# Kernel optimization log

Measured on AMD Instinct MI355X. Metric: run time of the kernel, lower is better.

Reference implementation:

```python
import jax, jax.numpy as jnp
import numpy as np

N_NODES = 100000
BN_EPS = 1e-5


def gcn_conv(x, row, col, ew, W, b, n):
    # PyG GCNConv (normalize=True, add_self_loops=True):
    # add self loops with weight 1, symmetric deg^-1/2 normalization,
    # message = norm * (x @ W)[row], scatter-add at col (target), + bias.
    h = x @ W  # [N, F_out]
    loop = jnp.arange(n)
    row_f = jnp.concatenate([row, loop])
    col_f = jnp.concatenate([col, loop])
    ew_f = jnp.concatenate([ew, jnp.ones((n,), dtype=ew.dtype)])
    deg = jax.ops.segment_sum(ew_f, col_f, num_segments=n)  # [N]
    dis = jnp.where(deg > 0, jax.lax.rsqrt(jnp.maximum(deg, 1e-30)), 0.0)
    norm = dis[row_f] * ew_f * dis[col_f]  # [E+N]
    msg = norm[:, None] * h[row_f]  # [E+N, F_out]
    agg = jax.ops.segment_sum(msg, col_f, num_segments=n)
    return agg + b


def batchnorm(h, gamma, beta):
    mean = h.mean(axis=0)
    var = h.var(axis=0)  # biased, as torch BN training-mode normalization
    return gamma * (h - mean) * jax.lax.rsqrt(var + BN_EPS) + beta


def setup_inputs() -> dict:
    key = jax.random.key(0)
    ks = jax.random.split(key, 12)
    N, E, D = N_NODES, 3200000, 256
    x = jax.random.normal(ks[0], (N, D), dtype=jnp.float32)
    edge_index = jax.random.randint(ks[1], (2, E), 0, N, dtype=jnp.int64)
    edge_weight = jax.random.uniform(ks[2], (E,), dtype=jnp.float32)
    s = 1.0 / np.sqrt(D)
    W1 = jax.random.uniform(ks[3], (D, D), jnp.float32, -s, s)
    b1 = jnp.zeros((D,), jnp.float32)
    g1 = jnp.ones((D,), jnp.float32)
    be1 = jnp.zeros((D,), jnp.float32)
    W2 = jax.random.uniform(ks[4], (D, D), jnp.float32, -s, s)
    b2 = jnp.zeros((D,), jnp.float32)
    g2 = jnp.ones((D,), jnp.float32)
    be2 = jnp.zeros((D,), jnp.float32)
    return {"x": x, "edge_index": edge_index, "edge_weight": edge_weight,
            "W1": W1, "b1": b1, "g1": g1, "be1": be1,
            "W2": W2, "b2": b2, "g2": g2, "be2": be2}


def reference(x, edge_index, edge_weight, W1, b1, g1, be1, W2, b2, g2, be2):
    n = x.shape[0]
    row, col = edge_index[0], edge_index[1]
    h = gcn_conv(x, row, col, edge_weight, W1, b1, n)
    h = jax.nn.relu(batchnorm(h, g1, be1))
    h = gcn_conv(h, row, col, edge_weight, W2, b2, n)
    h = batchnorm(h, g2, be2)
    # in_dim == out_dim -> proj is Identity
    return jax.nn.relu(h + x)
```

## Files before the change

### kernel.cpp

```cpp
#include <hip/hip_runtime.h>
#include <hip/hip_bf16.h>

#define D 256
#define BN_EPS 1e-5f
#define CHUNK 4096
#define NPB 512
#define CAP_B 20480

typedef __attribute__((ext_vector_type(8))) short bf16x8;
typedef __attribute__((ext_vector_type(4))) float f32x4;
typedef unsigned long long ull;
typedef unsigned char uchar;

__device__ inline uint pack2_rne(float a, float b) {
    uint ua = __builtin_bit_cast(uint, a);
    ua = ua + 0x7FFFu + ((ua >> 16) & 1u);
    uint ub = __builtin_bit_cast(uint, b);
    ub = ub + 0x7FFFu + ((ub >> 16) & 1u);
    return (ua >> 16) | (ub & 0xFFFF0000u);
}
__device__ inline ushort f2bf_rne(float a) {
    uint ua = __builtin_bit_cast(uint, a);
    ua = ua + 0x7FFFu + ((ua >> 16) & 1u);
    return (ushort)(ua >> 16);
}
__device__ inline float bf2f(ushort u) {
    uint x = ((uint)u) << 16;
    return __builtin_bit_cast(float, x);
}
__device__ inline uint pack_edge(uint rowbits, uint ewbits) {
    uint b15 = (ewbits + 0x8000u) >> 16;
    return (rowbits & 0x1FFFFu) | (b15 << 17);
}
__device__ inline float edge_ew(uint e) {
    return __builtin_bit_cast(float, (e >> 17) << 16);
}

__global__ __launch_bounds__(256) void init_fast_kernel(int* __restrict__ cursor,
                                                        float* __restrict__ stats) {
    int t = threadIdx.x;
    cursor[t] = t * CAP_B;
    stats[t] = 0.f;
    stats[t + 256] = 0.f;
    stats[t + 512] = 0.f;
    stats[t + 768] = 0.f;
}

__global__ __launch_bounds__(256) void bin_kernel(const int* __restrict__ row,
                                                  const int* __restrict__ col,
                                                  const float* __restrict__ ew,
                                                  int* __restrict__ cursor,
                                                  uint2* __restrict__ bdata, int E) {
    __shared__ int h[256];
    __shared__ int base[256];
    int t = threadIdx.x;
    h[t] = 0;
    __syncthreads();
    int cb = blockIdx.x * CHUNK;
    int cols[CHUNK / 256];
#pragma unroll
    for (int i = 0; i < CHUNK / 256; ++i) {
        int e = cb + i * 256 + t;
        int c = (e < E) ? col[e] : -1;
        cols[i] = c;
        if (c >= 0) atomicAdd(&h[c >> 9], 1);
    }
    __syncthreads();
    if (h[t]) base[t] = atomicAdd(&cursor[t], h[t]);
    __syncthreads();
    h[t] = 0;
    __syncthreads();
#pragma unroll
    for (int i = 0; i < CHUNK / 256; ++i) {
        int e = cb + i * 256 + t;
        int c = cols[i];
        if (c >= 0) {
            int b = c >> 9;
            int pos = base[b] + atomicAdd(&h[b], 1);
            if (pos < (b + 1) * CAP_B) {
                uint xv = (uint)row[e] | ((uint)(c & (NPB - 1)) << 17);
                bdata[pos] = make_uint2(xv, __float_as_uint(ew[e]));
            }
        }
    }
}

__global__ __launch_bounds__(256) void final_csr_kernel(const uint2* __restrict__ bdata,
                                                        const int* __restrict__ cursor,
                                                        uint* __restrict__ csr,
                                                        int* __restrict__ offs,
                                                        int* __restrict__ cnts,
                                                        float2* __restrict__ dscale, int N) {
    __shared__ int cnt[NPB];
    __shared__ float deg[NPB];
    __shared__ int sp[256];
    int bkt = blockIdx.x;
    int t = threadIdx.x;
    int beg = bkt * CAP_B;
    int end = min(cursor[bkt], beg + CAP_B);
    cnt[t] = 0; cnt[t + 256] = 0;
    deg[t] = 0.f; deg[t + 256] = 0.f;
    __syncthreads();
    for (int i = beg + t; i < end; i += 256) {
        uint2 v = bdata[i];
        int cl = v.x >> 17;
        atomicAdd(&cnt[cl], 1);
        atomicAdd(&deg[cl], __uint_as_float(v.y));
    }
    __syncthreads();
    int a0 = cnt[2 * t], a1 = cnt[2 * t + 1];
    sp[t] = a0 + a1;
    __syncthreads();
    for (int o = 1; o < 256; o <<= 1) {
        int add = (t >= o) ? sp[t - o] : 0;
        __syncthreads();
        sp[t] += add;
        __syncthreads();
    }
    int ex = sp[t] - (a0 + a1);
    int n0 = bkt * NPB + 2 * t;
    if (n0 < N) {
        offs[n0] = beg + ex;
        cnts[n0] = a0;
        dscale[n0].x = rsqrtf(deg[2 * t] + 1.0f);
    }
    if (n0 + 1 < N) {
        offs[n0 + 1] = beg + ex + a0;
        cnts[n0 + 1] = a1;
        dscale[n0 + 1].x = rsqrtf(deg[2 * t + 1] + 1.0f);
    }
    __syncthreads();
    cnt[2 * t] = ex;
    cnt[2 * t + 1] = ex + a0;
    __syncthreads();
    for (int i = beg + t; i < end; i += 256) {
        uint2 v = bdata[i];
        int cl = v.x >> 17;
        int pos = beg + atomicAdd(&cnt[cl], 1);
        csr[pos] = pack_edge(v.x, v.y);
    }
}

__global__ __launch_bounds__(256) void count_deg_kernel(const int* __restrict__ col,
                                                        const float* __restrict__ ew,
                                                        ull* __restrict__ dg, int E) {
    int e = blockIdx.x * 256 + threadIdx.x;
    if (e < E) {
        int c = col[e];
        uint q = (uint)(ew[e] * 8388608.0f + 0.5f);
        atomicAdd(&dg[c], (1ull << 40) | (ull)q);
    }
}

__global__ __launch_bounds__(256) void dis_cnt_kernel(const ull* __restrict__ dg,
                                                      float2* __restrict__ dscale,
                                                      int* __restrict__ cnt,
                                                      int* __restrict__ cnts,
                                                      float* __restrict__ stats, int N) {
    int i = blockIdx.x * 256 + threadIdx.x;
    if (i < 1024) stats[i] = 0.0f;
    if (i < N) {
        ull g = dg[i];
        int c = (int)(g >> 40);
        cnt[i] = c;
        cnts[i] = c;
        float deg = (float)(g & ((1ull << 40) - 1)) * (1.0f / 8388608.0f);
        dscale[i].x = rsqrtf(deg + 1.0f);
    }
}

__global__ __launch_bounds__(256) void scan_reduce(const int* __restrict__ cnt,
                                                   int* __restrict__ bsum, int N) {
    __shared__ int sd[256];
    int t = threadIdx.x;
    int i = blockIdx.x * 256 + t;
    sd[t] = (i < N) ? cnt[i] : 0;
    __syncthreads();
    for (int o = 128; o > 0; o >>= 1) {
        if (t < o) sd[t] += sd[t + o];
        __syncthreads();
    }
    if (t == 0) bsum[blockIdx.x] = sd[0];
}

__global__ __launch_bounds__(512) void scan_bsum(int* __restrict__ bsum, int B) {
    __shared__ int sd[512];
    int t = threadIdx.x;
    int v = (t < B) ? bsum[t] : 0;
    sd[t] = v;
    __syncthreads();
    for (int o = 1; o < 512; o <<= 1) {
        int add = (t >= o) ? sd[t - o] : 0;
        __syncthreads();
        sd[t] += add;
        __syncthreads();
    }
    if (t < B) bsum[t] = sd[t] - v;
}

__global__ __launch_bounds__(256) void scan_final(const int* __restrict__ cnt,
                                                  const int* __restrict__ bsum,
                                                  int* __restrict__ offs,
                                                  int* __restrict__ next, int N, int E) {
    __shared__ int sd[256];
    int t = threadIdx.x;
    int i = blockIdx.x * 256 + t;
    int v = (i < N) ? cnt[i] : 0;
    sd[t] = v;
    __syncthreads();
    for (int o = 1; o < 256; o <<= 1) {
        int add = (t >= o) ? sd[t - o] : 0;
        __syncthreads();
        sd[t] += add;
        __syncthreads();
    }
    int excl = sd[t] - v + bsum[blockIdx.x];
    if (i < N) {
        offs[i] = excl;
        next[i] = excl;
    }
    if (i == 0 && blockIdx.x == 0) offs[N] = E;
}

__global__ __launch_bounds__(256) void fill_kernel(const int* __restrict__ row,
                                                   const int* __restrict__ col,
                                                   const float* __restrict__ ew,
                                                   int* __restrict__ next,
                                                   uint* __restrict__ csr, int E) {
    int e = blockIdx.x * 256 + threadIdx.x;
    if (e < E) {
        int pos = atomicAdd(&next[col[e]], 1);
        csr[pos] = pack_edge((uint)row[e], __float_as_uint(ew[e]));
    }
}

__global__ __launch_bounds__(256) void prep_wt2_kernel(const float* __restrict__ W1,
                                                       const float* __restrict__ W2,
                                                       ushort* __restrict__ Wt1,
                                                       ushort* __restrict__ Wt2) {
    __shared__ float tile[64][65];
    const float* W = blockIdx.y ? W2 : W1;
    ushort* Wt = blockIdx.y ? Wt2 : Wt1;
    int t = threadIdx.x;
    int k0 = (blockIdx.x >> 2) * 64;
    int n0 = (blockIdx.x & 3) * 64;
#pragma unroll
    for (int it = 0; it < 16; ++it) {
        int idx = it * 256 + t;
        int r = idx >> 6, c = idx & 63;
        tile[r][c] = W[(size_t)(k0 + r) * D + n0 + c];
    }
    __syncthreads();
#pragma unroll
    for (int it = 0; it < 16; ++it) {
        int idx = it * 256 + t;
        int n = idx >> 6, k = idx & 63;
        Wt[(size_t)(n0 + n) * D + k0 + k] = f2bf_rne(tile[k][n]);
    }
}

template <int MODE>
__global__ __launch_bounds__(256) void gemm_mfma(const float* __restrict__ Xf,
                                                 const ushort* __restrict__ Xb,
                                                 const float* __restrict__ stats,
                                                 const float* __restrict__ gamma,
                                                 const float* __restrict__ beta,
                                                 const ushort* __restrict__ Wt,
                                                 uchar* __restrict__ Hq,
                                                 float2* __restrict__ dscale,
                                                 int N, float invN) {
    __shared__ char wt_lds[32 * 1024];
    __shared__ float cf_lds[2][MODE ? 256 : 1];
    const int t = threadIdx.x;
    const int wv = t >> 6;
    const int l = t & 63;
    const int ln = l & 15;
    const int kg0 = l >> 4;
    const int rblk = blockIdx.x * 128 + wv * 32;

    if constexpr (MODE == 1) {
        float mean = stats[t] * invN;
        float var = fmaxf(stats[D + t] * invN - mean * mean, 0.0f);
        float sc = gamma[t] * rsqrtf(var + BN_EPS);
        cf_lds[0][t] = sc;
        cf_lds[1][t] = beta[t] - sc * mean;
    }

    f32x4 acc[2][16];
#pragma unroll
    for (int g = 0; g < 2; ++g)
#pragma unroll
        for (int i = 0; i < 16; ++i) acc[g][i] = f32x4{0.f, 0.f, 0.f, 0.f};

    const int sg_n = t >> 3;
    const int sg_g = t & 7;
    const int sg_lds = (sg_g ^ (sg_n & 7)) * 16;

    for (int kt = 0; kt < 4; ++kt) {
        const int k0 = kt * 64;
        __syncthreads();
#pragma unroll
        for (int p = 0; p < 8; ++p) {
            int n = p * 32 + sg_n;
            uint4 v = *reinterpret_cast<const uint4*>(Wt + (size_t)n * 256 + k0 + sg_g * 8);
            *reinterpret_cast<uint4*>(&wt_lds[n * 128 + sg_lds]) = v;
        }
        __syncthreads();
#pragma unroll
        for (int kh = 0; kh < 2; ++kh) {
            const int kb = k0 + kh * 32 + kg0 * 8;
            bf16x8 afr[2];
#pragma unroll
            for (int g = 0; g < 2; ++g) {
                int arow = rblk + g * 16 + ln;
                afr[g] = bf16x8{};
                if (arow < N) {
                    if constexpr (MODE == 0) {
                        const float* ap = Xf + (size_t)arow * D + kb;
                        float4 f0 = *reinterpret_cast<const float4*>(ap);
                        float4 f1 = *reinterpret_cast<const float4*>(ap + 4);
                        uint4 u;
                        u.x = (__builtin_bit_cast(uint, f0.x) >> 16) | (__builtin_bit_cast(uint, f0.y) & 0xFFFF0000u);
                        u.y = (__builtin_bit_cast(uint, f0.z) >> 16) | (__builtin_bit_cast(uint, f0.w) & 0xFFFF0000u);
                        u.z = (__builtin_bit_cast(uint, f1.x) >> 16) | (__builtin_bit_cast(uint, f1.y) & 0xFFFF0000u);
                        u.w = (__builtin_bit_cast(uint, f1.z) >> 16) | (__builtin_bit_cast(uint, f1.w) & 0xFFFF0000u);
                        afr[g] = __builtin_bit_cast(bf16x8, u);
                    } else {
                        bf16x8 raw = *reinterpret_cast<const bf16x8*>(Xb + (size_t)arow * D + kb);
                        f32x4 scA = *reinterpret_cast<const f32x4*>(&cf_lds[0][kb]);
                        f32x4 scB = *reinterpret_cast<const f32x4*>(&cf_lds[0][kb + 4]);
                        f32x4 shA = *reinterpret_cast<const f32x4*>(&cf_lds[1][kb]);
                        f32x4 shB = *reinterpret_cast<const f32x4*>(&cf_lds[1][kb + 4]);
                        uint4 u;
                        u.x = pack2_rne(fmaxf(scA[0] * bf2f((ushort)raw[0]) + shA[0], 0.f),
                                        fmaxf(scA[1] * bf2f((ushort)raw[1]) + shA[1], 0.f));
                        u.y = pack2_rne(fmaxf(scA[2] * bf2f((ushort)raw[2]) + shA[2], 0.f),
                                        fmaxf(scA[3] * bf2f((ushort)raw[3]) + shA[3], 0.f));
                        u.z = pack2_rne(fmaxf(scB[0] * bf2f((ushort)raw[4]) + shB[0], 0.f),
                                        fmaxf(scB[1] * bf2f((ushort)raw[5]) + shB[1], 0.f));
                        u.w = pack2_rne(fmaxf(scB[2] * bf2f((ushort)raw[6]) + shB[2], 0.f),
                                        fmaxf(scB[3] * bf2f((ushort)raw[7]) + shB[3], 0.f));
                        afr[g] = __builtin_bit_cast(bf16x8, u);
                    }
                }
            }
            const int s = ln * 128 + (((kg0 + kh * 4) ^ (ln & 7)) * 16);
            const char* bbase = &wt_lds[s];
#pragma unroll
            for (int ct = 0; ct < 16; ++ct) {
                bf16x8 bfr = *reinterpret_cast<const bf16x8*>(bbase + ct * 2048);
                acc[0][ct] = __builtin_amdgcn_mfma_f32_16x16x32_bf16(afr[0], bfr, acc[0][ct], 0, 0, 0);
                acc[1][ct] = __builtin_amdgcn_mfma_f32_16x16x32_bf16(afr[1], bfr, acc[1][ct], 0, 0, 0);
            }
        }
    }

    __syncthreads();
    uchar* qtile = (uchar*)wt_lds;
#pragma unroll
    for (int g = 0; g < 2; ++g) {
#pragma unroll
        for (int r = 0; r < 4; ++r) {
            float am = 0.f;
#pragma unroll
            for (int ct = 0; ct < 16; ++ct) am = fmaxf(am, fabsf(acc[g][ct][r]));
#pragma unroll
            for (int mk = 1; mk < 16; mk <<= 1) am = fmaxf(am, __shfl_xor(am, mk));
            float qs = am > 0.f ? 127.0f / am : 0.f;
            int rloc = wv * 32 + g * 16 + kg0 * 4 + r;
            int rowi = blockIdx.x * 128 + rloc;
            if (ln == 0 && rowi < N) dscale[rowi].y = am * (1.0f / 127.0f);
#pragma unroll
            for (int ct = 0; ct < 16; ++ct) {
                int q = (int)rintf(acc[g][ct][r] * qs) + 128;
                qtile[rloc * 256 + ct * 16 + ln] = (uchar)q;
            }
        }
    }
    __syncthreads();
    const uint4* qt4 = reinterpret_cast<const uint4*>(qtile);
#pragma unroll
    for (int k = 0; k < 8; ++k) {
        int j = k * 256 + t;
        int rowi = blockIdx.x * 128 + (j >> 4);
        if (rowi < N)
            *reinterpret_cast<uint4*>(Hq + (size_t)rowi * 256 + (j & 15) * 16) = qt4[j];
    }
}

__global__ __launch_bounds__(256) void gather_q_kernel(const uchar* __restrict__ hq,
                                                       ushort* __restrict__ ha,
                                                       const uint* __restrict__ csr,
                                                       const int* __restrict__ offs,
                                                       const int* __restrict__ cnts,
                                                       const float2* __restrict__ dscale,
                                                       int N) {
    int wv = threadIdx.x >> 6;
    int lane = threadIdx.x & 63;
    int node = blockIdx.x * 4 + wv;
    if (node >= N) return;
    int beg = offs[node];
    int cnt = cnts[node];
    float2 dsn = dscale[node];
    float dc = dsn.x;
    int g = lane >> 4;
    int u = lane & 15;

    float acc[16];
#pragma unroll
    for (int j = 0; j < 16; ++j) acc[j] = 0.f;
    float S = 0.f;

    int total = cnt + 1;
    for (int base = 0; base < total; base += 64) {
        int m = min(64, total - base);
        int gi = base + lane;
        int r = node;
        float w = 0.f;
        if (gi < cnt) {
            uint v = __builtin_nontemporal_load(csr + beg + gi);
            r = (int)(v & 0x1FFFFu);
            float2 dsr = dscale[r];
            w = edge_ew(v) * dsr.x * dc * dsr.y;
        } else if (gi == cnt) {
            w = dc * dc * dsn.y;
        }
        S += w;
        for (int i = 0; i < m; i += 4) {
            int src = i + g;
            int er = __shfl(r, src);
            float we = __shfl(w, src);
            uint4 q = *reinterpret_cast<const uint4*>(hq + (size_t)er * 256 + u * 16);
#pragma unroll
            for (int b = 0; b < 4; ++b) {
                uint qq = (&q.x)[b];
                acc[b * 4 + 0] = fmaf(we, (float)(qq & 0xFF), acc[b * 4 + 0]);
                acc[b * 4 + 1] = fmaf(we, (float)((qq >> 8) & 0xFF), acc[b * 4 + 1]);
                acc[b * 4 + 2] = fmaf(we, (float)((qq >> 16) & 0xFF), acc[b * 4 + 2]);
                acc[b * 4 + 3] = fmaf(we, (float)(qq >> 24), acc[b * 4 + 3]);
            }
        }
    }

#pragma unroll
    for (int j = 0; j < 16; ++j) {
        float a = acc[j];
        a += __shfl_xor(a, 16);
        a += __shfl_xor(a, 32);
        acc[j] = a;
    }
#pragma unroll
    for (int mk = 1; mk < 64; mk <<= 1) S += __shfl_xor(S, mk);

    if (g == 0) {
        float c = 128.0f * S;
        uint o[8];
#pragma unroll
        for (int j = 0; j < 8; ++j)
            o[j] = pack2_rne(acc[2 * j] - c, acc[2 * j + 1] - c);
        uint4* dst = reinterpret_cast<uint4*>(ha + (size_t)node * D + u * 16);
        dst[0] = make_uint4(o[0], o[1], o[2], o[3]);
        dst[1] = make_uint4(o[4], o[5], o[6], o[7]);
    }
}

__global__ __launch_bounds__(256) void stats_bf16_kernel(const ushort* __restrict__ ha,
                                                         float* __restrict__ stats, int N) {
    __shared__ float ls[512];
    int t = threadIdx.x;
    int tq = t & 63;
    int tr = t >> 6;
    float s[4] = {0.f, 0.f, 0.f, 0.f};
    float q[4] = {0.f, 0.f, 0.f, 0.f};
    for (int i = blockIdx.x * 4 + tr; i < N; i += gridDim.x * 4) {
        uint2 u = *reinterpret_cast<const uint2*>(ha + (size_t)i * D + tq * 4);
        float v0 = bf2f((ushort)u.x), v1 = bf2f((ushort)(u.x >> 16));
        float v2 = bf2f((ushort)u.y), v3 = bf2f((ushort)(u.y >> 16));
        s[0] += v0; q[0] += v0 * v0;
        s[1] += v1; q[1] += v1 * v1;
        s[2] += v2; q[2] += v2 * v2;
        s[3] += v3; q[3] += v3 * v3;
    }
    ls[t] = 0.f; ls[t + 256] = 0.f;
    __syncthreads();
#pragma unroll
    for (int j = 0; j < 4; ++j) {
        int c = tq * 4 + j;
        atomicAdd(&ls[c], s[j]);
        atomicAdd(&ls[256 + c], q[j]);
    }
    __syncthreads();
    for (int i = t; i < 512; i += 256)
        unsafeAtomicAdd(&stats[i], ls[i]);
}

__global__ __launch_bounds__(256) void final_kernel(const ushort* __restrict__ ha,
                                                    const float* __restrict__ x,
                                                    const float* __restrict__ stats2,
                                                    const float* __restrict__ gamma,
                                                    const float* __restrict__ beta,
                                                    float* __restrict__ out,
                                                    int N, float invN) {
    __shared__ float cf[2][256];
    int t = threadIdx.x;
    {
        float mean = stats2[t] * invN;
        float var = fmaxf(stats2[D + t] * invN - mean * mean, 0.0f);
        float sc = gamma[t] * rsqrtf(var + BN_EPS);
        cf[0][t] = sc;
        cf[1][t] = beta[t] - sc * mean;
    }
    __syncthreads();
    size_t i = (size_t)blockIdx.x * 256 + t;
    size_t total = (size_t)N * (D / 4);
    if (i >= total) return;
    int c0 = (int)((i * 4) & (D - 1));
    uint2 h = reinterpret_cast<const uint2*>(ha)[i];
    f32x4 xv = *(reinterpret_cast<const f32x4*>(x) + i);
    f32x4 sc4 = *reinterpret_cast<const f32x4*>(&cf[0][c0]);
    f32x4 sh4 = *reinterpret_cast<const f32x4*>(&cf[1][c0]);
    f32x4 o;
    o[0] = fmaxf(sc4[0] * bf2f((ushort)h.x) + sh4[0] + xv[0], 0.0f);
    o[1] = fmaxf(sc4[1] * bf2f((ushort)(h.x >> 16)) + sh4[1] + xv[1], 0.0f);
    o[2] = fmaxf(sc4[2] * bf2f((ushort)h.y) + sh4[2] + xv[2], 0.0f);
    o[3] = fmaxf(sc4[3] * bf2f((ushort)(h.y >> 16)) + sh4[3] + xv[3], 0.0f);
    __builtin_nontemporal_store(o, reinterpret_cast<f32x4*>(out) + i);
}

extern "C" void kernel_launch(void* const* d_in, const int* in_sizes, int n_in,
                              void* d_out, int out_size, void* d_ws, size_t ws_size,
                              hipStream_t stream) {
    const float* x  = (const float*)d_in[0];
    const int* eidx = (const int*)d_in[1];
    const float* ew = (const float*)d_in[2];
    const float* W1 = (const float*)d_in[3];
    const float* g1  = (const float*)d_in[5];
    const float* be1 = (const float*)d_in[6];
    const float* W2  = (const float*)d_in[7];
    const float* g2  = (const float*)d_in[9];
    const float* be2 = (const float*)d_in[10];
    float* out = (float*)d_out;

    const int N = in_sizes[0] / D;
    const int E = in_sizes[2];
    const int* row = eidx;
    const int* col = eidx + E;
    const float invN = 1.0f / (float)N;

    uchar* hq    = (uchar*)d_ws;
    ushort* ha   = (ushort*)(hq + (size_t)N * 256);
    ushort* Wt1  = ha + (size_t)N * D;
    ushort* Wt2  = Wt1 + 65536;
    float* stats = (float*)(Wt2 + 65536);
    float2* dscale = (float2*)(stats + 1024);
    int*   offs  = (int*)(dscale + N);
    int*   cnts  = offs + (N + 1);

    size_t head = (size_t)N * 256 + (size_t)N * D * 2 + (size_t)65536 * 4 + 1024 * 4
                + (size_t)N * 8 + (size_t)(N + 1) * 4 + (size_t)N * 4;

    const int nb = (N + NPB - 1) / NPB;
    const int nchunk = (E + CHUNK - 1) / CHUNK;
    const int scanB = (N + 255) / 256;
    const int gemmB = (N + 127) / 128;
    const int gElems4 = (N * (D / 4) + 255) / 256;

    size_t need_fast = head + 256 * 4 + 16 + (size_t)nb * CAP_B * 12;
    const bool fast = (N < (1 << 17)) && (nb <= 256) && (ws_size >= need_fast)
                   && ((size_t)nb * CAP_B >= (size_t)E);

    uint* csr;

    if (fast) {
        int* cursor = cnts + N;
        uintptr_t p = ((uintptr_t)(cursor + 256) + 15) & ~(uintptr_t)15;
        uint2* bdata = (uint2*)p;
        csr = (uint*)(bdata + (size_t)nb * CAP_B);

        init_fast_kernel<<<1, 256, 0, stream>>>(cursor, stats);
        bin_kernel<<<nchunk, 256, 0, stream>>>(row, col, ew, cursor, bdata, E);
        final_csr_kernel<<<nb, 256, 0, stream>>>(bdata, cursor, csr, offs, cnts, dscale, N);
    } else {
        int* cntnext = cnts + N;
        ull* dg   = (ull*)(cntnext + N);
        int* bsum = (int*)dg;
        csr = (uint*)(dg + N);
        hipMemsetAsync(dg, 0, (size_t)N * 8, stream);
        count_deg_kernel<<<(E + 255) / 256, 256, 0, stream>>>(col, ew, dg, E);
        dis_cnt_kernel<<<scanB, 256, 0, stream>>>(dg, dscale, cntnext, cnts, stats, N);
        scan_reduce<<<scanB, 256, 0, stream>>>(cntnext, bsum, N);
        scan_bsum<<<1, 512, 0, stream>>>(bsum, scanB);
        scan_final<<<scanB, 256, 0, stream>>>(cntnext, bsum, offs, cntnext, N, E);
        fill_kernel<<<(E + 255) / 256, 256, 0, stream>>>(row, col, ew, cntnext, csr, E);
    }

    prep_wt2_kernel<<<dim3(16, 2), 256, 0, stream>>>(W1, W2, Wt1, Wt2);

    const int gatherB = (N + 3) / 4;

    gemm_mfma<0><<<gemmB, 256, 0, stream>>>(x, nullptr, nullptr, nullptr, nullptr,
                                            Wt1, hq, dscale, N, invN);
    gather_q_kernel<<<gatherB, 256, 0, stream>>>(hq, ha, csr, offs, cnts, dscale, N);
    stats_bf16_kernel<<<1024, 256, 0, stream>>>(ha, stats, N);

    gemm_mfma<1><<<gemmB, 256, 0, stream>>>(nullptr, ha, stats, g1, be1,
                                            Wt2, hq, dscale, N, invN);
    gather_q_kernel<<<gatherB, 256, 0, stream>>>(hq, ha, csr, offs, cnts, dscale, N);
    stats_bf16_kernel<<<1024, 256, 0, stream>>>(ha, stats + 512, N);

    final_kernel<<<gElems4, 256, 0, stream>>>(ha, x, stats + 512, g2, be2, out, N, invN);
}
```

Baseline: 599.0 us.

## Precompute per-source scale product and restructure gather to per-group edge loads

The GEMM epilogue now writes a combined per-row factor (dis times quantization scale) into a separate array, so the gather reads one float per source instead of a float2. The gather loop drops the 64-wide cooperative edge load plus shuffles: each 16-lane group now loads its own edge and row scale directly, unrolled by two. Init work is folded into the weight-transpose kernel to save a launch. The trade is more redundant csr/dprod loads per lane in place of the shuffle overhead.

```diff
diff --git a/kernel.cpp b/kernel.cpp
--- a/kernel.cpp
+++ b/kernel.cpp
@@ -36,14 +36,39 @@
     return __builtin_bit_cast(float, (e >> 17) << 16);
 }
 
-__global__ __launch_bounds__(256) void init_fast_kernel(int* __restrict__ cursor,
-                                                        float* __restrict__ stats) {
-    int t = threadIdx.x;
-    cursor[t] = t * CAP_B;
-    stats[t] = 0.f;
-    stats[t + 256] = 0.f;
-    stats[t + 512] = 0.f;
-    stats[t + 768] = 0.f;
+__global__ __launch_bounds__(256) void prep_wt2_kernel(const float* __restrict__ W1,
+                                                       const float* __restrict__ W2,
+                                                       ushort* __restrict__ Wt1,
+                                                       ushort* __restrict__ Wt2,
+                                                       int* __restrict__ cursor,
+                                                       float* __restrict__ stats,
+                                                       int doInit) {
+    __shared__ float tile[64][65];
+    int t = threadIdx.x;
+    if (doInit && blockIdx.x == 0 && blockIdx.y == 0) {
+        cursor[t] = t * CAP_B;
+        stats[t] = 0.f;
+        stats[t + 256] = 0.f;
+        stats[t + 512] = 0.f;
+        stats[t + 768] = 0.f;
+    }
+    const float* W = blockIdx.y ? W2 : W1;
+    ushort* Wt = blockIdx.y ? Wt2 : Wt1;
+    int k0 = (blockIdx.x >> 2) * 64;
+    int n0 = (blockIdx.x & 3) * 64;
+#pragma unroll
+    for (int it = 0; it < 16; ++it) {
+        int idx = it * 256 + t;
+        int r = idx >> 6, c = idx & 63;
+        tile[r][c] = W[(size_t)(k0 + r) * D + n0 + c];
+    }
+    __syncthreads();
+#pragma unroll
+    for (int it = 0; it < 16; ++it) {
+        int idx = it * 256 + t;
+        int n = idx >> 6, k = idx & 63;
+        Wt[(size_t)(n0 + n) * D + k0 + k] = f2bf_rne(tile[k][n]);
+    }
 }
 
 __global__ __launch_bounds__(256) void bin_kernel(const int* __restrict__ row,
@@ -90,7 +115,7 @@
                                                         uint* __restrict__ csr,
                                                         int* __restrict__ offs,
                                                         int* __restrict__ cnts,
-                                                        float2* __restrict__ dscale, int N) {
+                                                        float* __restrict__ dis, int N) {
     __shared__ int cnt[NPB];
     __shared__ float deg[NPB];
     __shared__ int sp[256];
@@ -122,12 +147,12 @@
     if (n0 < N) {
         offs[n0] = beg + ex;
         cnts[n0] = a0;
-        dscale[n0].x = rsqrtf(deg[2 * t] + 1.0f);
+        dis[n0] = rsqrtf(deg[2 * t] + 1.0f);
     }
     if (n0 + 1 < N) {
         offs[n0 + 1] = beg + ex + a0;
         cnts[n0 + 1] = a1;
-        dscale[n0 + 1].x = rsqrtf(deg[2 * t + 1] + 1.0f);
+        dis[n0 + 1] = rsqrtf(deg[2 * t + 1] + 1.0f);
     }
     __syncthreads();
     cnt[2 * t] = ex;
@@ -153,7 +178,7 @@
 }
 
 __global__ __launch_bounds__(256) void dis_cnt_kernel(const ull* __restrict__ dg,
-                                                      float2* __restrict__ dscale,
+                                                      float* __restrict__ dis,
                                                       int* __restrict__ cnt,
                                                       int* __restrict__ cnts,
                                                       float* __restrict__ stats, int N) {
@@ -165,7 +190,7 @@
         cnt[i] = c;
         cnts[i] = c;
         float deg = (float)(g & ((1ull << 40) - 1)) * (1.0f / 8388608.0f);
-        dscale[i].x = rsqrtf(deg + 1.0f);
+        dis[i] = rsqrtf(deg + 1.0f);
     }
 }
 
@@ -234,31 +259,6 @@
     }
 }
 
-__global__ __launch_bounds__(256) void prep_wt2_kernel(const float* __restrict__ W1,
-                                                       const float* __restrict__ W2,
-                                                       ushort* __restrict__ Wt1,
-                                                       ushort* __restrict__ Wt2) {
-    __shared__ float tile[64][65];
-    const float* W = blockIdx.y ? W2 : W1;
-    ushort* Wt = blockIdx.y ? Wt2 : Wt1;
-    int t = threadIdx.x;
-    int k0 = (blockIdx.x >> 2) * 64;
-    int n0 = (blockIdx.x & 3) * 64;
-#pragma unroll
-    for (int it = 0; it < 16; ++it) {
-        int idx = it * 256 + t;
-        int r = idx >> 6, c = idx & 63;
-        tile[r][c] = W[(size_t)(k0 + r) * D + n0 + c];
-    }
-    __syncthreads();
-#pragma unroll
-    for (int it = 0; it < 16; ++it) {
-        int idx = it * 256 + t;
-        int n = idx >> 6, k = idx & 63;
-        Wt[(size_t)(n0 + n) * D + k0 + k] = f2bf_rne(tile[k][n]);
-    }
-}
-
 template <int MODE>
 __global__ __launch_bounds__(256) void gemm_mfma(const float* __restrict__ Xf,
                                                  const ushort* __restrict__ Xb,
@@ -267,7 +267,8 @@
                                                  const float* __restrict__ beta,
                                                  const ushort* __restrict__ Wt,
                                                  uchar* __restrict__ Hq,
-                                                 float2* __restrict__ dscale,
+                                                 const float* __restrict__ dis,
+                                                 float* __restrict__ dprod,
                                                  int N, float invN) {
     __shared__ char wt_lds[32 * 1024];
     __shared__ float cf_lds[2][MODE ? 256 : 1];
@@ -369,7 +370,8 @@
             float qs = am > 0.f ? 127.0f / am : 0.f;
             int rloc = wv * 32 + g * 16 + kg0 * 4 + r;
             int rowi = blockIdx.x * 128 + rloc;
-            if (ln == 0 && rowi < N) dscale[rowi].y = am * (1.0f / 127.0f);
+            if (ln == 0 && rowi < N)
+                dprod[rowi] = dis[rowi] * (am * (1.0f / 127.0f));
 #pragma unroll
             for (int ct = 0; ct < 16; ++ct) {
                 int q = (int)rintf(acc[g][ct][r] * qs) + 128;
@@ -393,7 +395,8 @@
                                                        const uint* __restrict__ csr,
                                                        const int* __restrict__ offs,
                                                        const int* __restrict__ cnts,
-                                                       const float2* __restrict__ dscale,
+                                                       const float* __restrict__ dis,
+                                                       const float* __restrict__ dprod,
                                                        int N) {
     int wv = threadIdx.x >> 6;
     int lane = threadIdx.x & 63;
@@ -401,8 +404,7 @@
     if (node >= N) return;
     int beg = offs[node];
     int cnt = cnts[node];
-    float2 dsn = dscale[node];
-    float dc = dsn.x;
+    float dc = dis[node];
     int g = lane >> 4;
     int u = lane & 15;
 
@@ -412,33 +414,27 @@
     float S = 0.f;
 
     int total = cnt + 1;
-    for (int base = 0; base < total; base += 64) {
-        int m = min(64, total - base);
-        int gi = base + lane;
+#pragma unroll 2
+    for (int base = 0; base < total; base += 4) {
+        int gi = base + g;
         int r = node;
         float w = 0.f;
         if (gi < cnt) {
             uint v = __builtin_nontemporal_load(csr + beg + gi);
             r = (int)(v & 0x1FFFFu);
-            float2 dsr = dscale[r];
-            w = edge_ew(v) * dsr.x * dc * dsr.y;
+            w = edge_ew(v) * dprod[r] * dc;
         } else if (gi == cnt) {
-            w = dc * dc * dsn.y;
+            w = dc * dprod[node];
         }
-        S += w;
-        for (int i = 0; i < m; i += 4) {
-            int src = i + g;
-            int er = __shfl(r, src);
-            float we = __shfl(w, src);
-            uint4 q = *reinterpret_cast<const uint4*>(hq + (size_t)er * 256 + u * 16);
-#pragma unroll
-            for (int b = 0; b < 4; ++b) {
-                uint qq = (&q.x)[b];
-                acc[b * 4 + 0] = fmaf(we, (float)(qq & 0xFF), acc[b * 4 + 0]);
-                acc[b * 4 + 1] = fmaf(we, (float)((qq >> 8) & 0xFF), acc[b * 4 + 1]);
-                acc[b * 4 + 2] = fmaf(we, (float)((qq >> 16) & 0xFF), acc[b * 4 + 2]);
-                acc[b * 4 + 3] = fmaf(we, (float)(qq >> 24), acc[b * 4 + 3]);
-            }
+        uint4 q = *reinterpret_cast<const uint4*>(hq + (size_t)r * 256 + u * 16);
+        if (u == 0) S += w;
+#pragma unroll
+        for (int b = 0; b < 4; ++b) {
+            uint qq = (&q.x)[b];
+            acc[b * 4 + 0] = fmaf(w, (float)(qq & 0xFF), acc[b * 4 + 0]);
+            acc[b * 4 + 1] = fmaf(w, (float)((qq >> 8) & 0xFF), acc[b * 4 + 1]);
+            acc[b * 4 + 2] = fmaf(w, (float)((qq >> 16) & 0xFF), acc[b * 4 + 2]);
+            acc[b * 4 + 3] = fmaf(w, (float)(qq >> 24), acc[b * 4 + 3]);
         }
     }
 
@@ -552,8 +548,9 @@
     ushort* Wt1  = ha + (size_t)N * D;
     ushort* Wt2  = Wt1 + 65536;
     float* stats = (float*)(Wt2 + 65536);
-    float2* dscale = (float2*)(stats + 1024);
-    int*   offs  = (int*)(dscale + N);
+    float* dis   = stats + 1024;
+    float* dprod = dis + N;
+    int*   offs  = (int*)(dprod + N);
     int*   cnts  = offs + (N + 1);
 
     size_t head = (size_t)N * 256 + (size_t)N * D * 2 + (size_t)65536 * 4 + 1024 * 4
@@ -577,9 +574,10 @@
         uint2* bdata = (uint2*)p;
         csr = (uint*)(bdata + (size_t)nb * CAP_B);
 
-        init_fast_kernel<<<1, 256, 0, stream>>>(cursor, stats);
+        prep_wt2_kernel<<<dim3(16, 2), 256, 0, stream>>>(W1, W2, Wt1, Wt2,
+                                                         cursor, stats, 1);
         bin_kernel<<<nchunk, 256, 0, stream>>>(row, col, ew, cursor, bdata, E);
-        final_csr_kernel<<<nb, 256, 0, stream>>>(bdata, cursor, csr, offs, cnts, dscale, N);
+        final_csr_kernel<<<nb, 256, 0, stream>>>(bdata, cursor, csr, offs, cnts, dis, N);
     } else {
         int* cntnext = cnts + N;
         ull* dg   = (ull*)(cntnext + N);
@@ -587,25 +585,25 @@
         csr = (uint*)(dg + N);
         hipMemsetAsync(dg, 0, (size_t)N * 8, stream);
         count_deg_kernel<<<(E + 255) / 256, 256, 0, stream>>>(col, ew, dg, E);
-        dis_cnt_kernel<<<scanB, 256, 0, stream>>>(dg, dscale, cntnext, cnts, stats, N);
+        dis_cnt_kernel<<<scanB, 256, 0, stream>>>(dg, dis, cntnext, cnts, stats, N);
         scan_reduce<<<scanB, 256, 0, stream>>>(cntnext, bsum, N);
         scan_bsum<<<1, 512, 0, stream>>>(bsum, scanB);
         scan_final<<<scanB, 256, 0, stream>>>(cntnext, bsum, offs, cntnext, N, E);
         fill_kernel<<<(E + 255) / 256, 256, 0, stream>>>(row, col, ew, cntnext, csr, E);
-    }
-
-    prep_wt2_kernel<<<dim3(16, 2), 256, 0, stream>>>(W1, W2, Wt1, Wt2);
+        prep_wt2_kernel<<<dim3(16, 2), 256, 0, stream>>>(W1, W2, Wt1, Wt2,
+                                                         nullptr, stats, 0);
+    }
 
     const int gatherB = (N + 3) / 4;
 
     gemm_mfma<0><<<gemmB, 256, 0, stream>>>(x, nullptr, nullptr, nullptr, nullptr,
-                                            Wt1, hq, dscale, N, invN);
-    gather_q_kernel<<<gatherB, 256, 0, stream>>>(hq, ha, csr, offs, cnts, dscale, N);
+                                            Wt1, hq, dis, dprod, N, invN);
+    gather_q_kernel<<<gatherB, 256, 0, stream>>>(hq, ha, csr, offs, cnts, dis, dprod, N);
     stats_bf16_kernel<<<1024, 256, 0, stream>>>(ha, stats, N);
 
     gemm_mfma<1><<<gemmB, 256, 0, stream>>>(nullptr, ha, stats, g1, be1,
-                                            Wt2, hq, dscale, N, invN);
-    gather_q_kernel<<<gatherB, 256, 0, stream>>>(hq, ha, csr, offs, cnts, dscale, N);
+                                            Wt2, hq, dis, dprod, N, invN);
+    gather_q_kernel<<<gatherB, 256, 0, stream>>>(hq, ha, csr, offs, cnts, dis, dprod, N);
     stats_bf16_kernel<<<1024, 256, 0, stream>>>(ha, stats + 512, N);
 
     final_kernel<<<gElems4, 256, 0, stream>>>(ha, x, stats + 512, g2, be2, out, N, invN);
```

Result: slower. 699.8 us (+16.8%).
